# Performance work log

Measured on AMD Instinct MI355X. Metric: run time of the kernel, lower is better.

## Reference

```python
import jax, jax.numpy as jnp
import numpy as np

B, S, F, D = 4, 1024, 8, 512
H = 8
DK = D // H
DF = 2048
ECLIPSE_BOOST = 2.0
LN_EPS = 1e-5


def _layer_norm(x, g, b):
    m = jnp.mean(x, axis=-1, keepdims=True)
    v = jnp.mean(jnp.square(x - m), axis=-1, keepdims=True)
    return (x - m) * jax.lax.rsqrt(v + LN_EPS) * g + b


def setup_inputs() -> dict:
    key = jax.random.key(0)
    ks = jax.random.split(key, 16)
    def lin_w(k, out_d, in_d):
        return jax.random.normal(k, (out_d, in_d), jnp.float32) * (1.0 / np.sqrt(in_d))
    return {
        "x": jax.random.normal(ks[0], (B, S, F, D), jnp.float32),
        "eclipse_mask": jax.random.bernoulli(ks[1], 0.3, (B, S)),
        "wq": lin_w(ks[2], D, D), "bq": jnp.zeros((D,), jnp.float32),
        "wk": lin_w(ks[3], D, D), "bk": jnp.zeros((D,), jnp.float32),
        "wv": lin_w(ks[4], D, D), "bv": jnp.zeros((D,), jnp.float32),
        "wo": lin_w(ks[5], D, D), "bo": jnp.zeros((D,), jnp.float32),
        "w1": lin_w(ks[6], DF, D), "b1": jnp.zeros((DF,), jnp.float32),
        "w2": lin_w(ks[7], D, DF), "b2": jnp.zeros((D,), jnp.float32),
        "g1": jnp.ones((D,), jnp.float32), "be1": jnp.zeros((D,), jnp.float32),
        "g2": jnp.ones((D,), jnp.float32), "be2": jnp.zeros((D,), jnp.float32),
    }


def reference(x, eclipse_mask, wq, bq, wk, bk, wv, bv, wo, bo, w1, b1, w2, b2, g1, be1, g2, be2):
    BF = B * F
    scale = 1.0 / np.sqrt(DK)
    # NOTE: the torch module does x.view(B*F, S, D) on a [B,S,F,D] tensor —
    # a raw memory reshape (NOT a transpose). Replicate exactly.
    xr = x.reshape(BF, S, D)  # [BF, S, D]
    # eclipse_mask [B,S] -> expand over features -> [BF, S] (rows b*F+f share mask[b])
    em = jnp.broadcast_to(eclipse_mask[:, None, :], (B, F, S)).reshape(BF, S)

    def proj(w, b):
        return (xr @ w.T + b).reshape(BF, S, H, DK).transpose(0, 2, 1, 3)  # [BF,H,S,DK]

    Q, K, V = proj(wq, bq), proj(wk, bk), proj(wv, bv)
    scores = jnp.einsum("bhqd,bhkd->bhqk", Q, K) * scale  # [BF,H,S,S]
    boost = jnp.where(em, ECLIPSE_BOOST, 1.0)[:, None, None, :]  # over key positions
    scores = scores * boost
    attn = jax.nn.softmax(scores, axis=-1)
    ctx = jnp.einsum("bhqk,bhkd->bhqd", attn, V)  # [BF,H,S,DK]
    ctx = ctx.transpose(0, 2, 1, 3).reshape(BF, S, D)
    attn_out = (ctx @ wo.T + bo).reshape(B, S, F, D)  # raw reshape back, matches torch

    h = _layer_norm(x + attn_out, g1, be1)
    ff = jax.nn.gelu(h @ w1.T + b1, approximate=False) @ w2.T + b2
    return _layer_norm(h + ff, g2, be2)
```

## Files before the change

kernel.cpp:

```cpp
#include <hip/hip_runtime.h>
#include <math.h>

typedef _Float16 half8 __attribute__((ext_vector_type(8)));
typedef float f32x4 __attribute__((ext_vector_type(4)));
typedef unsigned int u32;

#define AS1 __attribute__((address_space(1)))
#define AS3 __attribute__((address_space(3)))

__device__ __forceinline__ void g2lds16(const void* g, void* l) {
    __builtin_amdgcn_global_load_lds((const AS1 u32*)g, (AS3 u32*)l, 16, 0, 0);
}

__global__ __launch_bounds__(256)
void cvt_all(const float* __restrict__ x, const float* __restrict__ wq,
             const float* __restrict__ wk, const float* __restrict__ wv,
             const float* __restrict__ wo, const float* __restrict__ w1,
             const float* __restrict__ w2, _Float16* __restrict__ xh,
             _Float16* __restrict__ qkvw, _Float16* __restrict__ woh,
             _Float16* __restrict__ w1h, _Float16* __restrict__ w2h)
{
    const int bid = blockIdx.x;
    const float* src; _Float16* dst; int g;
    if (bid < 8192)      { src = x;  dst = xh;            g = bid*256 + threadIdx.x; }
    else if (bid < 8320) { src = wq; dst = qkvw;          g = (bid-8192)*256 + threadIdx.x; }
    else if (bid < 8448) { src = wk; dst = qkvw + 262144; g = (bid-8320)*256 + threadIdx.x; }
    else if (bid < 8576) { src = wv; dst = qkvw + 524288; g = (bid-8448)*256 + threadIdx.x; }
    else if (bid < 8704) { src = wo; dst = woh;           g = (bid-8576)*256 + threadIdx.x; }
    else if (bid < 9216) { src = w1; dst = w1h;           g = (bid-8704)*256 + threadIdx.x; }
    else                 { src = w2; dst = w2h;           g = (bid-9216)*256 + threadIdx.x; }
    const float4* p = (const float4*)src + (size_t)g * 2;
    float4 a = p[0], b = p[1];
    half8 h;
    h[0]=(_Float16)a.x; h[1]=(_Float16)a.y; h[2]=(_Float16)a.z; h[3]=(_Float16)a.w;
    h[4]=(_Float16)b.x; h[5]=(_Float16)b.y; h[6]=(_Float16)b.z; h[7]=(_Float16)b.w;
    *((half8*)dst + g) = h;
}

__global__ __launch_bounds__(256)
void pack_bias(const float* __restrict__ bq, const float* __restrict__ bk,
               const float* __restrict__ bv, float* __restrict__ o)
{
    const int i = blockIdx.x * 256 + threadIdx.x;
    o[i] = i < 512 ? bq[i] : (i < 1024 ? bk[i-512] : bv[i-1024]);
}

template<int MODE>
__global__ __launch_bounds__(256)
void gemm_bt(const _Float16* __restrict__ A, const _Float16* __restrict__ B,
             const float* __restrict__ bias, const float* __restrict__ resf,
             const _Float16* __restrict__ resh, void* __restrict__ Cout,
             int M, int N, int K)
{
    __shared__ __align__(16) _Float16 As[128 * 32];
    __shared__ __align__(16) _Float16 Bs[128 * 32];
    const int tid = threadIdx.x;
    const int lane = tid & 63;
    const int w = tid >> 6;
    const int wm = w >> 1, wn = w & 1;
    const int m0 = blockIdx.y * 128, n0 = blockIdx.x * 128;
    const int lrow = lane & 15;
    const int lk = (lane >> 4) * 8;

    f32x4 acc[4][4];
#pragma unroll
    for (int i = 0; i < 4; ++i)
#pragma unroll
        for (int j = 0; j < 4; ++j) acc[i][j] = (f32x4)0.0f;

    for (int k0 = 0; k0 < K; k0 += 32) {
#pragma unroll
        for (int i = 0; i < 2; ++i) {
            int gbase = i * 256 + w * 64;
            int g = gbase + lane;
            g2lds16(A + (size_t)(m0 + (g >> 2)) * K + k0 + (g & 3) * 8,
                    (char*)As + (size_t)gbase * 16);
            g2lds16(B + (size_t)(n0 + (g >> 2)) * K + k0 + (g & 3) * 8,
                    (char*)Bs + (size_t)gbase * 16);
        }
        __syncthreads();
        half8 af[4], bfr[4];
#pragma unroll
        for (int t = 0; t < 4; ++t) {
            af[t]  = *(const half8*)(As + (wm * 64 + t * 16 + lrow) * 32 + lk);
            bfr[t] = *(const half8*)(Bs + (wn * 64 + t * 16 + lrow) * 32 + lk);
        }
#pragma unroll
        for (int mi = 0; mi < 4; ++mi)
#pragma unroll
            for (int ni = 0; ni < 4; ++ni)
                acc[mi][ni] = __builtin_amdgcn_mfma_f32_16x16x32_f16(af[mi], bfr[ni], acc[mi][ni], 0, 0, 0);
        __syncthreads();
    }

    const int rq = (lane >> 4) * 4;
#pragma unroll
    for (int mi = 0; mi < 4; ++mi) {
#pragma unroll
        for (int ni = 0; ni < 4; ++ni) {
            const int col = n0 + wn * 64 + ni * 16 + lrow;
            const float bv = bias[col];
#pragma unroll
            for (int r = 0; r < 4; ++r) {
                const int row = m0 + wm * 64 + mi * 16 + rq + r;
                const size_t idx = (size_t)row * N + col;
                float v = acc[mi][ni][r] + bv;
                if (MODE == 0) {
                    ((_Float16*)Cout)[idx] = (_Float16)v;
                } else if (MODE == 1) {
                    float t2 = -1.5957691216057308f * v * fmaf(v * v, 0.044715f, 1.0f);
                    float e = __expf(t2);
                    ((_Float16*)Cout)[idx] = (_Float16)(v * __builtin_amdgcn_rcpf(1.0f + e));
                } else if (MODE == 2) {
                    ((float*)Cout)[idx] = v + resf[idx];
                } else {
                    ((float*)Cout)[idx] = v + (float)resh[idx];
                }
            }
        }
    }
}

__global__ __launch_bounds__(256)
void attn_fwd(const _Float16* __restrict__ QKV, const int* __restrict__ mask,
              _Float16* __restrict__ ctx)
{
    constexpr int SQ = 72;
    __shared__ __align__(16) _Float16 Ks[64 * SQ];
    __shared__ __align__(16) _Float16 Vts[64 * SQ];
    __shared__ __align__(16) _Float16 Ps[4][32 * SQ];
    __shared__ float scs[1024];

    const int tid = threadIdx.x;
    const int lane = tid & 63;
    const int w = tid >> 6;
    const int bf = blockIdx.y >> 3;
    const int hh = blockIdx.y & 7;
    const int q0 = blockIdx.x * 128;
    const int lrow = lane & 15;
    const int lq = lane >> 4;

    {
        const int* mrow = mask + (bf >> 3) * 1024;
        const int i = tid * 4;
        int4 mm = *(const int4*)(mrow + i);
        scs[i + 0] = mm.x ? 0.25f : 0.125f;
        scs[i + 1] = mm.y ? 0.25f : 0.125f;
        scs[i + 2] = mm.z ? 0.25f : 0.125f;
        scs[i + 3] = mm.w ? 0.25f : 0.125f;
    }

    half8 qf[2][2];
#pragma unroll
    for (int qi = 0; qi < 2; ++qi) {
        const _Float16* qp = QKV + (size_t)(bf * 1024 + q0 + w * 32 + qi * 16 + lrow) * 1536 + hh * 64 + lq * 8;
        qf[qi][0] = *(const half8*)qp;
        qf[qi][1] = *(const half8*)(qp + 32);
    }

    const _Float16* Kbase = QKV + (size_t)bf * 1024 * 1536 + 512 + hh * 64;
    const _Float16* Vbase = Kbase + 512;

    f32x4 acc[2][4];
#pragma unroll
    for (int qi = 0; qi < 2; ++qi)
#pragma unroll
        for (int d = 0; d < 4; ++d) acc[qi][d] = (f32x4)0.0f;
    float lpart[2][4] = {{0.f,0.f,0.f,0.f},{0.f,0.f,0.f,0.f}};
    _Float16* Pw = &Ps[w][0];

    for (int kt = 0; kt < 1024; kt += 64) {
        __syncthreads();
        {
            const int r = tid >> 3, c = (tid & 7) * 8;
            *(uint4*)&Ks[r * SQ + c]        = *(const uint4*)(Kbase + (size_t)(kt + r) * 1536 + c);
            *(uint4*)&Ks[(r + 32) * SQ + c] = *(const uint4*)(Kbase + (size_t)(kt + r + 32) * 1536 + c);
            const int key = lane, dvb = w * 16;
            const _Float16* vp = Vbase + (size_t)(kt + key) * 1536 + dvb;
            half8 v0 = *(const half8*)vp;
            half8 v1 = *(const half8*)(vp + 8);
#pragma unroll
            for (int j = 0; j < 8; ++j) Vts[(dvb + j) * SQ + key] = v0[j];
#pragma unroll
            for (int j = 0; j < 8; ++j) Vts[(dvb + 8 + j) * SQ + key] = v1[j];
        }
        __syncthreads();

#pragma unroll
        for (int nt = 0; nt < 4; ++nt) {
            half8 kf0 = *(const half8*)(Ks + (nt * 16 + lrow) * SQ + lq * 8);
            half8 kf1 = *(const half8*)(Ks + (nt * 16 + lrow) * SQ + 32 + lq * 8);
            const float sc = scs[kt + nt * 16 + lrow];
#pragma unroll
            for (int qi = 0; qi < 2; ++qi) {
                f32x4 s = (f32x4)0.0f;
                s = __builtin_amdgcn_mfma_f32_16x16x32_f16(qf[qi][0], kf0, s, 0, 0, 0);
                s = __builtin_amdgcn_mfma_f32_16x16x32_f16(qf[qi][1], kf1, s, 0, 0, 0);
#pragma unroll
                for (int r = 0; r < 4; ++r) {
                    float p = __expf(fmaf(s[r], sc, -5.0f));
                    lpart[qi][r] += p;
                    Pw[(qi * 16 + lq * 4 + r) * SQ + nt * 16 + lrow] = (_Float16)p;
                }
            }
        }

        half8 pf[2][2];
#pragma unroll
        for (int qi = 0; qi < 2; ++qi) {
            pf[qi][0] = *(const half8*)(Pw + (qi * 16 + lrow) * SQ + lq * 8);
            pf[qi][1] = *(const half8*)(Pw + (qi * 16 + lrow) * SQ + 32 + lq * 8);
        }
#pragma unroll
        for (int d = 0; d < 4; ++d) {
            half8 vf0 = *(const half8*)(Vts + (d * 16 + lrow) * SQ + lq * 8);
            half8 vf1 = *(const half8*)(Vts + (d * 16 + lrow) * SQ + 32 + lq * 8);
#pragma unroll
            for (int qi = 0; qi < 2; ++qi) {
                acc[qi][d] = __builtin_amdgcn_mfma_f32_16x16x32_f16(pf[qi][0], vf0, acc[qi][d], 0, 0, 0);
                acc[qi][d] = __builtin_amdgcn_mfma_f32_16x16x32_f16(pf[qi][1], vf1, acc[qi][d], 0, 0, 0);
            }
        }
    }

#pragma unroll
    for (int qi = 0; qi < 2; ++qi) {
#pragma unroll
        for (int r = 0; r < 4; ++r) {
            float l = lpart[qi][r];
            l += __shfl_xor(l, 1); l += __shfl_xor(l, 2);
            l += __shfl_xor(l, 4); l += __shfl_xor(l, 8);
            const float inv = 1.0f / l;
            const int row = q0 + w * 32 + qi * 16 + lq * 4 + r;
            _Float16* cp = ctx + ((size_t)bf * 1024 + row) * 512 + hh * 64;
#pragma unroll
            for (int d = 0; d < 4; ++d)
                cp[d * 16 + lrow] = (_Float16)(acc[qi][d][r] * inv);
        }
    }
}

template<int OUTH>
__global__ __launch_bounds__(256)
void ln_fused(const float* __restrict__ X, const float* __restrict__ gma,
              const float* __restrict__ bta, float* __restrict__ outF,
              _Float16* __restrict__ outH)
{
    const int row = blockIdx.x * 4 + (threadIdx.x >> 6);
    const int lane = threadIdx.x & 63;
    const float4* xr = (const float4*)(X + (size_t)row * 512);
    float4 a = xr[lane * 2], c = xr[lane * 2 + 1];
    float s  = a.x + a.y + a.z + a.w + c.x + c.y + c.z + c.w;
    float s2 = a.x * a.x + a.y * a.y + a.z * a.z + a.w * a.w
             + c.x * c.x + c.y * c.y + c.z * c.z + c.w * c.w;
#pragma unroll
    for (int m = 1; m < 64; m <<= 1) { s += __shfl_xor(s, m); s2 += __shfl_xor(s2, m); }
    const float mean = s * (1.0f / 512.0f);
    const float inv = rsqrtf(s2 * (1.0f / 512.0f) - mean * mean + 1e-5f);
    const float4* gp = (const float4*)gma;
    const float4* bp = (const float4*)bta;
    float4 g0 = gp[lane * 2], g1 = gp[lane * 2 + 1];
    float4 b0 = bp[lane * 2], b1 = bp[lane * 2 + 1];
    float4 o0, o1;
    o0.x = (a.x - mean) * inv * g0.x + b0.x; o0.y = (a.y - mean) * inv * g0.y + b0.y;
    o0.z = (a.z - mean) * inv * g0.z + b0.z; o0.w = (a.w - mean) * inv * g0.w + b0.w;
    o1.x = (c.x - mean) * inv * g1.x + b1.x; o1.y = (c.y - mean) * inv * g1.y + b1.y;
    o1.z = (c.z - mean) * inv * g1.z + b1.z; o1.w = (c.w - mean) * inv * g1.w + b1.w;
    if (OUTH) {
        half8 hv;
        hv[0] = (_Float16)o0.x; hv[1] = (_Float16)o0.y; hv[2] = (_Float16)o0.z; hv[3] = (_Float16)o0.w;
        hv[4] = (_Float16)o1.x; hv[5] = (_Float16)o1.y; hv[6] = (_Float16)o1.z; hv[7] = (_Float16)o1.w;
        *((half8*)(outH + (size_t)row * 512) + lane) = hv;
    } else {
        float4* op = (float4*)(outF + (size_t)row * 512);
        op[lane * 2] = o0; op[lane * 2 + 1] = o1;
    }
}

extern "C" void kernel_launch(void* const* d_in, const int* in_sizes, int n_in,
                              void* d_out, int out_size, void* d_ws, size_t ws_size,
                              hipStream_t stream)
{
    const float* x   = (const float*)d_in[0];
    const int* mask  = (const int*)d_in[1];
    const float* wq  = (const float*)d_in[2];  const float* bq  = (const float*)d_in[3];
    const float* wk  = (const float*)d_in[4];  const float* bk  = (const float*)d_in[5];
    const float* wv  = (const float*)d_in[6];  const float* bv  = (const float*)d_in[7];
    const float* wo  = (const float*)d_in[8];  const float* bo  = (const float*)d_in[9];
    const float* w1  = (const float*)d_in[10]; const float* b1  = (const float*)d_in[11];
    const float* w2  = (const float*)d_in[12]; const float* b2  = (const float*)d_in[13];
    const float* g1  = (const float*)d_in[14]; const float* be1 = (const float*)d_in[15];
    const float* g2  = (const float*)d_in[16]; const float* be2 = (const float*)d_in[17];
    float* out = (float*)d_out;

    char* ws = (char*)d_ws;
    _Float16* qkvh = (_Float16*)(ws);
    _Float16* ctxh = (_Float16*)(ws + 100663296);
    _Float16* gh   = (_Float16*)(ws);
    _Float16* xh   = (_Float16*)(ws + 134217728);
    float*    res  = (float*)   (ws + 134217728);
    _Float16* hhb  = (_Float16*)(ws + 201326592);
    float*    biasf= (float*)   (ws + 201326592);
    _Float16* qkvw = (_Float16*)(ws + 234881024);
    _Float16* woh  = (_Float16*)(ws + 236453888);
    _Float16* w1h  = (_Float16*)(ws + 236978176);
    _Float16* w2h  = (_Float16*)(ws + 239075328);

    dim3 blk(256);

    cvt_all<<<9728, blk, 0, stream>>>(x, wq, wk, wv, wo, w1, w2, xh, qkvw, woh, w1h, w2h);
    pack_bias<<<6, blk, 0, stream>>>(bq, bk, bv, biasf);

    gemm_bt<0><<<dim3(12, 256), blk, 0, stream>>>(xh, qkvw, biasf, nullptr, nullptr, qkvh, 32768, 1536, 512);

    attn_fwd<<<dim3(8, 256), blk, 0, stream>>>(qkvh, mask, ctxh);

    gemm_bt<2><<<dim3(4, 256), blk, 0, stream>>>(ctxh, woh, bo, x, nullptr, res, 32768, 512, 512);

    ln_fused<1><<<8192, blk, 0, stream>>>(res, g1, be1, nullptr, hhb);

    gemm_bt<1><<<dim3(16, 256), blk, 0, stream>>>(hhb, w1h, b1, nullptr, nullptr, gh, 32768, 2048, 512);

    gemm_bt<3><<<dim3(4, 256), blk, 0, stream>>>(gh, w2h, b2, nullptr, hhb, res, 32768, 512, 2048);

    ln_fused<0><<<8192, blk, 0, stream>>>(res, g2, be2, out, nullptr);
}
```

Baseline: 696.5 us.

## Load GEMM fragments directly from global with register double-buffering and XCD-aware tile mapping

Removes the LDS staging and both block-wide barriers from the GEMM main loop. Each wave now loads its MFMA fragments straight from global memory into registers, prefetching the next K-slice while computing the current one. Block indices are also remapped so that consecutive M tiles land on the same XCD, which should improve L2 reuse. The cost is that tiles are no longer shared through LDS, so each A/B row is fetched by two waves and global traffic goes up. The mapping also assumes gridDim.y is a power-of-two multiple of 8.

Result: slower. 1.048 ms (+50.5%).

```diff
diff --git a/kernel.cpp b/kernel.cpp
--- a/kernel.cpp
+++ b/kernel.cpp
@@ -52,46 +52,59 @@
              const _Float16* __restrict__ resh, void* __restrict__ Cout,
              int M, int N, int K)
 {
-    __shared__ __align__(16) _Float16 As[128 * 32];
-    __shared__ __align__(16) _Float16 Bs[128 * 32];
     const int tid = threadIdx.x;
     const int lane = tid & 63;
     const int w = tid >> 6;
     const int wm = w >> 1, wn = w & 1;
-    const int m0 = blockIdx.y * 128, n0 = blockIdx.x * 128;
+
+    const int bid = blockIdx.x + gridDim.x * blockIdx.y;
+    const int nyc = gridDim.y >> 3;
+    const int xcd = bid & 7;
+    const int chunk = bid >> 3;
+    const int m_blk = xcd * nyc + (chunk & (nyc - 1));
+    const int n_blk = chunk / nyc;
+    const int m0 = m_blk * 128, n0 = n_blk * 128;
+
     const int lrow = lane & 15;
     const int lk = (lane >> 4) * 8;
 
+    const _Float16* Ap = A + (size_t)(m0 + wm * 64 + lrow) * K + lk;
+    const _Float16* Bp = B + (size_t)(n0 + wn * 64 + lrow) * K + lk;
+    const size_t rstep = (size_t)16 * K;
+
     f32x4 acc[4][4];
 #pragma unroll
     for (int i = 0; i < 4; ++i)
 #pragma unroll
         for (int j = 0; j < 4; ++j) acc[i][j] = (f32x4)0.0f;
 
-    for (int k0 = 0; k0 < K; k0 += 32) {
-#pragma unroll
-        for (int i = 0; i < 2; ++i) {
-            int gbase = i * 256 + w * 64;
-            int g = gbase + lane;
-            g2lds16(A + (size_t)(m0 + (g >> 2)) * K + k0 + (g & 3) * 8,
-                    (char*)As + (size_t)gbase * 16);
-            g2lds16(B + (size_t)(n0 + (g >> 2)) * K + k0 + (g & 3) * 8,
-                    (char*)Bs + (size_t)gbase * 16);
-        }
-        __syncthreads();
-        half8 af[4], bfr[4];
+    half8 a0[4], b0[4];
+#pragma unroll
+    for (int t = 0; t < 4; ++t) {
+        a0[t] = *(const half8*)(Ap + t * rstep);
+        b0[t] = *(const half8*)(Bp + t * rstep);
+    }
+
+    for (int k0 = 32; k0 < K; k0 += 32) {
+        half8 a1[4], b1[4];
 #pragma unroll
         for (int t = 0; t < 4; ++t) {
-            af[t]  = *(const half8*)(As + (wm * 64 + t * 16 + lrow) * 32 + lk);
-            bfr[t] = *(const half8*)(Bs + (wn * 64 + t * 16 + lrow) * 32 + lk);
+            a1[t] = *(const half8*)(Ap + t * rstep + k0);
+            b1[t] = *(const half8*)(Bp + t * rstep + k0);
         }
 #pragma unroll
         for (int mi = 0; mi < 4; ++mi)
 #pragma unroll
             for (int ni = 0; ni < 4; ++ni)
-                acc[mi][ni] = __builtin_amdgcn_mfma_f32_16x16x32_f16(af[mi], bfr[ni], acc[mi][ni], 0, 0, 0);
-        __syncthreads();
-    }
+                acc[mi][ni] = __builtin_amdgcn_mfma_f32_16x16x32_f16(a0[mi], b0[ni], acc[mi][ni], 0, 0, 0);
+#pragma unroll
+        for (int t = 0; t < 4; ++t) { a0[t] = a1[t]; b0[t] = b1[t]; }
+    }
+#pragma unroll
+    for (int mi = 0; mi < 4; ++mi)
+#pragma unroll
+        for (int ni = 0; ni < 4; ++ni)
+            acc[mi][ni] = __builtin_amdgcn_mfma_f32_16x16x32_f16(a0[mi], b0[ni], acc[mi][ni], 0, 0, 0);
 
     const int rq = (lane >> 4) * 4;
 #pragma unroll
```
